# Kernel optimization log

Measured on AMD Instinct MI355X. Metric: run time of the kernel, lower is better.

## Reference

```python
import jax, jax.numpy as jnp
import numpy as np

N, E = 50000, 800000
DIM_IN, DIM_H, DIM_OUT, HEADS = 128, 32, 16, 4
HID = DIM_H * HEADS  # 128
FINAL = DIM_OUT * HEADS  # 64
NEG_SLOPE = 0.2


def _glorot(key, shape):
    fan_in, fan_out = shape[0], shape[-1] if len(shape) > 1 else shape[0]
    lim = jnp.sqrt(6.0 / (fan_in + fan_out)).astype(jnp.float32)
    return jax.random.uniform(key, shape, jnp.float32, -lim, lim)


def setup_inputs() -> dict:
    key = jax.random.key(0)
    ks = jax.random.split(key, 16)
    x = jax.random.normal(ks[0], (N, DIM_IN), jnp.float32)
    edge_index = jax.random.randint(ks[1], (2, E), 0, N, dtype=jnp.int64)
    inp = {"x": x, "edge_index": edge_index}
    # layer 1: DIM_IN -> HEADS*DIM_H
    inp["Wl1"] = _glorot(ks[2], (DIM_IN, HEADS * DIM_H))
    inp["Wr1"] = _glorot(ks[3], (DIM_IN, HEADS * DIM_H))
    inp["att1"] = _glorot(ks[4], (HEADS, DIM_H))
    inp["b1"] = jnp.zeros((HEADS * DIM_H,), jnp.float32)
    # layer 2: HID -> HEADS*DIM_H
    inp["Wl2"] = _glorot(ks[5], (HID, HEADS * DIM_H))
    inp["Wr2"] = _glorot(ks[6], (HID, HEADS * DIM_H))
    inp["att2"] = _glorot(ks[7], (HEADS, DIM_H))
    inp["b2"] = jnp.zeros((HEADS * DIM_H,), jnp.float32)
    # layer 3: HID -> HEADS*DIM_OUT
    inp["Wl3"] = _glorot(ks[8], (HID, HEADS * DIM_OUT))
    inp["Wr3"] = _glorot(ks[9], (HID, HEADS * DIM_OUT))
    inp["att3"] = _glorot(ks[10], (HEADS, DIM_OUT))
    inp["b3"] = jnp.zeros((HEADS * DIM_OUT,), jnp.float32)
    return inp


def gatv2_conv(x, src, dst, Wl, Wr, att, b, heads, ch):
    n = x.shape[0]
    xl = (x @ Wl).reshape(n, heads, ch)  # source-side transform
    xr = (x @ Wr).reshape(n, heads, ch)  # target-side transform
    m = xl[src] + xr[dst]                 # [E, H, C]
    e = jnp.einsum('ehc,hc->eh', jax.nn.leaky_relu(m, NEG_SLOPE), att)
    # segment softmax over incoming edges of each dst node
    emax = jax.ops.segment_max(e, dst, num_segments=n)
    ex = jnp.exp(e - emax[dst])
    denom = jax.ops.segment_sum(ex, dst, num_segments=n)
    alpha = ex / denom[dst]               # [E, H]
    out = jax.ops.segment_sum(alpha[:, :, None] * xl[src], dst, num_segments=n)
    return out.reshape(n, heads * ch) + b


def reference(x, edge_index, Wl1, Wr1, att1, b1, Wl2, Wr2, att2, b2, Wl3, Wr3, att3, b3):
    n = x.shape[0]
    loops = jnp.arange(n, dtype=edge_index.dtype)
    src = jnp.concatenate([edge_index[0], loops])  # PyG add_self_loops=True
    dst = jnp.concatenate([edge_index[1], loops])
    # dropout is identity in eval mode
    h = jax.nn.elu(gatv2_conv(x, src, dst, Wl1, Wr1, att1, b1, HEADS, DIM_H))
    h = jax.nn.elu(gatv2_conv(h, src, dst, Wl2, Wr2, att2, b2, HEADS, DIM_H))
    h = gatv2_conv(h, src, dst, Wl3, Wr3, att3, b3, HEADS, DIM_OUT)
    return jax.nn.log_softmax(h, axis=1)
```

## Files before the change

kernel.cpp:

```cpp
#include <hip/hip_runtime.h>
#include <math.h>

constexpr int DIN  = 128;
constexpr int FSH  = 8;
constexpr int NFBM = 200;
constexpr int LCAP = 72;
constexpr int RND  = 4096;
constexpr int FCAP = 4608;

typedef __attribute__((ext_vector_type(8))) short short8;
typedef __attribute__((ext_vector_type(4))) float f32x4;

__device__ __forceinline__ unsigned short f2bf(float f) {
  unsigned u = __float_as_uint(f);
  u = (u + 0x7FFF + ((u >> 16) & 1)) >> 16;
  return (unsigned short)u;
}
__device__ __forceinline__ float bflo(unsigned u) { return __uint_as_float(u << 16); }
__device__ __forceinline__ float bfhi(unsigned u) { return __uint_as_float(u & 0xFFFF0000u); }

__device__ __forceinline__ void unpack8(uint4 u, float* x) {
  x[0] = bflo(u.x); x[1] = bfhi(u.x); x[2] = bflo(u.y); x[3] = bfhi(u.y);
  x[4] = bflo(u.z); x[5] = bfhi(u.z); x[6] = bflo(u.w); x[7] = bfhi(u.w);
}
__device__ __forceinline__ void unpack4(uint2 u, float* x) {
  x[0] = bflo(u.x); x[1] = bfhi(u.x); x[2] = bflo(u.y); x[3] = bfhi(u.y);
}

typedef const __attribute__((address_space(1))) unsigned int guint_t;
typedef __attribute__((address_space(3))) unsigned int luint_t;
__device__ __forceinline__ void async16(const void* g, void* l) {
  __builtin_amdgcn_global_load_lds((guint_t*)g, (luint_t*)l, 16, 0, 0);
}


__global__ __launch_bounds__(256) void prep_kernel(const int* __restrict__ ei,
    int* __restrict__ gcnt, unsigned* __restrict__ gpairs, int E, int nfb, int appb,
    const float* __restrict__ Wl1, const float* __restrict__ Wr1,
    const float* __restrict__ Wl2, const float* __restrict__ Wr2,
    const float* __restrict__ Wl3, const float* __restrict__ Wr3,
    unsigned short* __restrict__ Wt) {
  __shared__ unsigned buf[NFBM * LCAP];
  __shared__ int cnt[NFBM];
  __shared__ int gbase[NFBM];
  const int tid = threadIdx.x;

  if (blockIdx.x >= appb) {
    int e = (blockIdx.x - appb) * 256 + tid;
    if (e >= 81920) return;
    const float* src; int N; int off;
    if (e < 65536) {
      int m = e >> 14; off = e & 16383; N = 128;
      src = (m == 0) ? Wl1 : (m == 1) ? Wr1 : (m == 2) ? Wl2 : Wr2;
    } else {
      int e2 = e - 65536; int m = e2 >> 13; off = e2 & 8191; N = 64;
      src = m ? Wr3 : Wl3;
    }
    int nn = off >> 7, k = off & 127;
    Wt[e] = f2bf(src[(size_t)k * N + nn]);
    return;
  }

  if (tid < NFBM) cnt[tid] = 0;
  __syncthreads();

  const int k0 = blockIdx.x * RND;
  for (int i = tid; i < RND; i += 256) {
    int k = k0 + i;
    if (k >= E) break;
    int src = ei[k], dst = ei[E + k];
    int fb = dst >> FSH;
    int pos = atomicAdd(&cnt[fb], 1);
    if (pos < LCAP)
      buf[fb * LCAP + pos] = (unsigned)src | ((unsigned)(dst & ((1 << FSH) - 1)) << 16);
  }
  __syncthreads();

  if (tid < nfb) gbase[tid] = atomicAdd(&gcnt[tid], min(cnt[tid], LCAP));
  __syncthreads();

  const int wid = tid >> 6, lane = tid & 63;
  for (int fb = wid; fb < nfb; fb += 4) {
    int c  = min(cnt[fb], LCAP);
    int gb = gbase[fb];
    if (gb >= FCAP) continue;
    c = min(c, FCAP - gb);
    unsigned* dstp = gpairs + (size_t)fb * FCAP + gb;
    const unsigned* srcp = &buf[fb * LCAP];
    for (int i = lane; i < c; i += 64) dstp[i] = srcp[i];
  }
}


struct BuildSmem { int hist[1 << FSH]; int wsum[4]; int base_s; };

__device__ __forceinline__ void build_body(BuildSmem& s, int b,
    const unsigned* __restrict__ gpairs, const int* __restrict__ gcnt,
    int* __restrict__ row_ptr, unsigned short* __restrict__ edge_src,
    int n, int nfb) {
  const int tid = threadIdx.x;
  const int lane = tid & 63, wid = tid >> 6;

  const int d0 = b << FSH;
  const int nvalid = min(1 << FSH, n - d0);

  if (wid == 0) {
    int term = 0;
    for (int i = lane; i < b; i += 64)
      term += min(gcnt[i], FCAP) + min(1 << FSH, n - (i << FSH));
#pragma unroll
    for (int o = 32; o >= 1; o >>= 1) term += __shfl_xor(term, o, 64);
    if (lane == 0) s.base_s = term;
  }
  s.hist[tid] = (tid < nvalid) ? 1 : 0;
  __syncthreads();

  const int cnt = min(gcnt[b], FCAP);
  const unsigned* bp = gpairs + (size_t)b * FCAP;
  for (int i = tid; i < cnt; i += 256)
    atomicAdd(&s.hist[bp[i] >> 16], 1);
  __syncthreads();

  const int h = s.hist[tid];
  int incl = h;
#pragma unroll
  for (int o = 1; o < 64; o <<= 1) {
    int t = __shfl_up(incl, o, 64);
    if (lane >= o) incl += t;
  }
  if (lane == 63) s.wsum[wid] = incl;
  __syncthreads();
  int wo = 0;
  for (int wq = 0; wq < wid; ++wq) wo += s.wsum[wq];
  const int base = s.base_s;
  const int excl = wo + incl - h;
  if (tid < nvalid) {
    row_ptr[d0 + tid] = base + excl;
    edge_src[base + excl] = (unsigned short)(d0 + tid);
    s.hist[tid] = excl + 1;
  } else if (d0 + tid == n) {
    row_ptr[n] = base + excl;
  }
  if (b == nfb - 1 && d0 + (1 << FSH) <= n && tid == 0)
    row_ptr[n] = base + cnt + nvalid;
  __syncthreads();

  for (int i = tid; i < cnt; i += 256) {
    unsigned p = bp[i];
    int pos = atomicAdd(&s.hist[p >> 16], 1);
    edge_src[base + pos] = (unsigned short)(p & 0xFFFFu);
  }
}


template<int NC, bool CVT>
__device__ __forceinline__ void gemm2_body(char* lds, int bid, const void* __restrict__ Ap,
    const unsigned short* __restrict__ Wlt, const unsigned short* __restrict__ Wrt,
    unsigned short* __restrict__ outl, unsigned short* __restrict__ outr, int M) {
  constexpr int WNB = NC / 16;
  char* As = lds;
  char* Ws = lds + 16384;
  const int tid  = threadIdx.x;
  const int w    = tid >> 6, lane = tid & 63;
  const int q    = lane >> 4, r15 = lane & 15;
  const int row0 = bid * 64;

  if constexpr (CVT) {
    const float* Af = (const float*)Ap;
    for (int idx = tid * 4; idx < 64 * 128; idx += 1024) {
      int rl = idx >> 7, k = idx & 127;
      int rg = row0 + rl; if (rg >= M) rg = M - 1;
      float4 v = *(const float4*)&Af[(size_t)rg * 128 + k];
      uint2 pk;
      pk.x = (unsigned)f2bf(v.x) | ((unsigned)f2bf(v.y) << 16);
      pk.y = (unsigned)f2bf(v.z) | ((unsigned)f2bf(v.w) << 16);
      char* addr = As + (rl >> 4) * 4096 + (k >> 5) * 1024 +
                   ((((k >> 3) & 3) * 16) + (rl & 15)) * 16 + (k & 7) * 2;
      *(uint2*)addr = pk;
    }
  } else {
    const unsigned short* A = (const unsigned short*)Ap;
    int r = row0 + w * 16 + r15; if (r >= M) r = M - 1;
    const char* g = (const char*)A + (size_t)r * 256 + q * 16;
    char* l = As + w * 4096;
#pragma unroll
    for (int kk = 0; kk < 4; ++kk) async16(g + kk * 64, l + kk * 1024);
  }
  for (int nt = w; nt < WNB; nt += 4) {
    const char* g = (const char*)Wlt + ((size_t)(nt * 16 + r15)) * 256 + q * 16;
    char* l = Ws + nt * 4096;
#pragma unroll
    for (int kk = 0; kk < 4; ++kk) async16(g + kk * 64, l + kk * 1024);
  }
  __syncthreads();

  const char* aw = As + w * 4096;
  f32x4 acc[WNB] = {};
#pragma unroll
  for (int kk = 0; kk < 4; ++kk) {
    short8 af = *(const short8*)(aw + kk * 1024 + (size_t)lane * 16);
#pragma unroll
    for (int nt = 0; nt < WNB; ++nt) {
      short8 bf = *(const short8*)(Ws + (nt * 4 + kk) * 1024 + (size_t)lane * 16);
      acc[nt] = __builtin_amdgcn_mfma_f32_16x16x32_bf16(af, bf, acc[nt], 0, 0, 0);
    }
  }
  {
    int rowb = row0 + w * 16 + q * 4;
#pragma unroll
    for (int nt = 0; nt < WNB; ++nt)
#pragma unroll
      for (int r = 0; r < 4; ++r) {
        int rr = rowb + r;
        if (rr < M) outl[(size_t)rr * NC + nt * 16 + r15] = f2bf(acc[nt][r]);
      }
  }
  __syncthreads();
  for (int nt = w; nt < WNB; nt += 4) {
    const char* g = (const char*)Wrt + ((size_t)(nt * 16 + r15)) * 256 + q * 16;
    char* l = Ws + nt * 4096;
#pragma unroll
    for (int kk = 0; kk < 4; ++kk) async16(g + kk * 64, l + kk * 1024);
  }
  __syncthreads();

  f32x4 acc2[WNB] = {};
#pragma unroll
  for (int kk = 0; kk < 4; ++kk) {
    short8 af = *(const short8*)(aw + kk * 1024 + (size_t)lane * 16);
#pragma unroll
    for (int nt = 0; nt < WNB; ++nt) {
      short8 bf = *(const short8*)(Ws + (nt * 4 + kk) * 1024 + (size_t)lane * 16);
      acc2[nt] = __builtin_amdgcn_mfma_f32_16x16x32_bf16(af, bf, acc2[nt], 0, 0, 0);
    }
  }
  {
    int rowb = row0 + w * 16 + q * 4;
#pragma unroll
    for (int nt = 0; nt < WNB; ++nt)
#pragma unroll
      for (int r = 0; r < 4; ++r) {
        int rr = rowb + r;
        if (rr < M) outr[(size_t)rr * NC + nt * 16 + r15] = f2bf(acc2[nt][r]);
      }
  }
}


union GemmBuildSmem { char lds[16384 + 128 * 256]; BuildSmem b; };

__global__ __launch_bounds__(256) void gemm1_build_kernel(const void* __restrict__ Ap,
    const unsigned short* __restrict__ Wlt, const unsigned short* __restrict__ Wrt,
    unsigned short* __restrict__ outl, unsigned short* __restrict__ outr,
    const unsigned* __restrict__ gpairs, const int* __restrict__ gcnt,
    int* __restrict__ row_ptr, unsigned short* __restrict__ edge_src,
    int n, int nfb) {
  __shared__ GemmBuildSmem smem;
  if (blockIdx.x < (unsigned)nfb)
    build_body(smem.b, blockIdx.x, gpairs, gcnt, row_ptr, edge_src, n, nfb);
  else
    gemm2_body<128, true>(smem.lds, blockIdx.x - nfb, Ap, Wlt, Wrt, outl, outr, n);
}


__device__ __forceinline__ uint4 agg128_node(
    const unsigned short* __restrict__ xl, const unsigned short* xr,
    const float* __restrict__ att, const float* __restrict__ bias,
    const int* __restrict__ row_ptr, const unsigned short* __restrict__ edge_src,
    int node, int c0) {
  float xrv[8];
  unpack8(*(const uint4*)&xr[(size_t)node * 128 + c0], xrv);
  float a6[8], a4[8];
  {
    float4 aa = *(const float4*)&att[c0];
    float4 ab = *(const float4*)&att[c0 + 4];
    float at[8] = {aa.x, aa.y, aa.z, aa.w, ab.x, ab.y, ab.z, ab.w};
#pragma unroll
    for (int j = 0; j < 8; ++j) { a6[j] = 0.6f * at[j]; a4[j] = 0.4f * at[j]; }
  }

  float l = 0.f, o[8] = {};
  int idx = row_ptr[node];
  const int end = row_ptr[node + 1];

  int s0 = 0, s1 = 0, s2 = 0, s3 = 0;
  if (idx + 4 <= end) {
    s0 = edge_src[idx];     s1 = edge_src[idx + 1];
    s2 = edge_src[idx + 2]; s3 = edge_src[idx + 3];
  }
  while (idx + 4 <= end) {
    uint4 u0 = *(const uint4*)&xl[(size_t)s0 * 128 + c0];
    uint4 u1 = *(const uint4*)&xl[(size_t)s1 * 128 + c0];
    uint4 u2 = *(const uint4*)&xl[(size_t)s2 * 128 + c0];
    uint4 u3 = *(const uint4*)&xl[(size_t)s3 * 128 + c0];
    idx += 4;
    if (idx + 4 <= end) {
      s0 = edge_src[idx];     s1 = edge_src[idx + 1];
      s2 = edge_src[idx + 2]; s3 = edge_src[idx + 3];
    }
    float x0[8], x1[8], x2[8], x3[8];
    unpack8(u0, x0); unpack8(u1, x1); unpack8(u2, x2); unpack8(u3, x3);
    float p0 = 0.f, p1 = 0.f, p2 = 0.f, p3 = 0.f;
#pragma unroll
    for (int j = 0; j < 8; ++j) {
      float t0 = x0[j] + xrv[j], t1 = x1[j] + xrv[j];
      float t2 = x2[j] + xrv[j], t3 = x3[j] + xrv[j];
      p0 = fmaf(t0, a6[j], p0); p0 = fmaf(fabsf(t0), a4[j], p0);
      p1 = fmaf(t1, a6[j], p1); p1 = fmaf(fabsf(t1), a4[j], p1);
      p2 = fmaf(t2, a6[j], p2); p2 = fmaf(fabsf(t2), a4[j], p2);
      p3 = fmaf(t3, a6[j], p3); p3 = fmaf(fabsf(t3), a4[j], p3);
    }
    p0 += __shfl_xor(p0, 1, 64); p0 += __shfl_xor(p0, 2, 64);
    p1 += __shfl_xor(p1, 1, 64); p1 += __shfl_xor(p1, 2, 64);
    p2 += __shfl_xor(p2, 1, 64); p2 += __shfl_xor(p2, 2, 64);
    p3 += __shfl_xor(p3, 1, 64); p3 += __shfl_xor(p3, 2, 64);
    float e0 = __expf(fminf(p0, 80.f)), e1 = __expf(fminf(p1, 80.f));
    float e2 = __expf(fminf(p2, 80.f)), e3 = __expf(fminf(p3, 80.f));
    l += (e0 + e1) + (e2 + e3);
#pragma unroll
    for (int j = 0; j < 8; ++j)
      o[j] = fmaf(e0, x0[j], fmaf(e1, x1[j], fmaf(e2, x2[j], fmaf(e3, x3[j], o[j]))));
  }
  for (; idx < end; ++idx) {
    int s = edge_src[idx];
    uint4 u0 = *(const uint4*)&xl[(size_t)s * 128 + c0];
    float x0[8];
    unpack8(u0, x0);
    float p0 = 0.f;
#pragma unroll
    for (int j = 0; j < 8; ++j) {
      float t = x0[j] + xrv[j];
      p0 = fmaf(t, a6[j], p0); p0 = fmaf(fabsf(t), a4[j], p0);
    }
    p0 += __shfl_xor(p0, 1, 64); p0 += __shfl_xor(p0, 2, 64);
    float e0 = __expf(fminf(p0, 80.f));
    l += e0;
#pragma unroll
    for (int j = 0; j < 8; ++j) o[j] = fmaf(e0, x0[j], o[j]);
  }

  float4 b0 = *(const float4*)&bias[c0];
  float4 b1 = *(const float4*)&bias[c0 + 4];
  float bb[8] = {b0.x, b0.y, b0.z, b0.w, b1.x, b1.y, b1.z, b1.w};
  float rl = 1.f / l;
  unsigned short res[8];
#pragma unroll
  for (int j = 0; j < 8; ++j) {
    float v = o[j] * rl + bb[j];
    v = v > 0.f ? v : __expf(v) - 1.f;
    res[j] = f2bf(v);
  }
  uint4 ov;
  ov.x = (unsigned)res[0] | ((unsigned)res[1] << 16);
  ov.y = (unsigned)res[2] | ((unsigned)res[3] << 16);
  ov.z = (unsigned)res[4] | ((unsigned)res[5] << 16);
  ov.w = (unsigned)res[6] | ((unsigned)res[7] << 16);
  return ov;
}


template<int NC>
__global__ __launch_bounds__(512, 4) void agg_gemm_kernel(
    const unsigned short* __restrict__ xg,
    const unsigned short* xr,
    const float* __restrict__ att, const float* __restrict__ bias,
    const int* __restrict__ row_ptr, const unsigned short* __restrict__ edge_src,
    const unsigned short* __restrict__ Wlt, const unsigned short* __restrict__ Wrt,
    unsigned short* outl, unsigned short* outr, int n) {
  constexpr int WNB = NC / 16;
  constexpr int NT2 = WNB / 2;
  __shared__ char lds[16384 + NC * 256];
  char* As = lds;
  char* Ws = lds + 16384;
  const int tid  = threadIdx.x;
  const int w8   = tid >> 6, lane = tid & 63;
  const int q    = lane >> 4, r15 = lane & 15;
  const int row0 = blockIdx.x * 64;

  for (int nt = w8; nt < WNB; nt += 8) {
    const char* g = (const char*)Wlt + ((size_t)(nt * 16 + r15)) * 256 + q * 16;
    char* l = Ws + nt * 4096;
#pragma unroll
    for (int kk = 0; kk < 4; ++kk) async16(g + kk * 64, l + kk * 1024);
  }

  const int r   = tid & 15;
  const int g16 = tid >> 4;
  const int c0  = r * 8;
#pragma unroll
  for (int pass = 0; pass < 2; ++pass) {
    const int rl   = pass * 32 + g16;
    const int node = row0 + rl;
    uint4 ov = make_uint4(0, 0, 0, 0);
    if (node < n)
      ov = agg128_node(xg, xr, att, bias, row_ptr, edge_src, node, c0);
    char* addr = As + (rl >> 4) * 4096 + (r >> 2) * 1024 +
                 (((r & 3) * 16) + (rl & 15)) * 16;
    *(uint4*)addr = ov;
  }
  __syncthreads();

  const int wq = w8 & 3;
  const int nh = w8 >> 2;
  const char* aw = As + wq * 4096;
  const int rowb = row0 + wq * 16 + q * 4;

  {
    f32x4 acc[NT2] = {};
#pragma unroll
    for (int kk = 0; kk < 4; ++kk) {
      short8 af = *(const short8*)(aw + kk * 1024 + (size_t)lane * 16);
#pragma unroll
      for (int t = 0; t < NT2; ++t) {
        short8 bf = *(const short8*)(Ws + ((nh * NT2 + t) * 4 + kk) * 1024 + (size_t)lane * 16);
        acc[t] = __builtin_amdgcn_mfma_f32_16x16x32_bf16(af, bf, acc[t], 0, 0, 0);
      }
    }
#pragma unroll
    for (int t = 0; t < NT2; ++t)
#pragma unroll
      for (int rr4 = 0; rr4 < 4; ++rr4) {
        int rr = rowb + rr4;
        if (rr < n) outl[(size_t)rr * NC + (nh * NT2 + t) * 16 + r15] = f2bf(acc[t][rr4]);
      }
  }
  __syncthreads();

  for (int nt = w8; nt < WNB; nt += 8) {
    const char* g = (const char*)Wrt + ((size_t)(nt * 16 + r15)) * 256 + q * 16;
    char* l = Ws + nt * 4096;
#pragma unroll
    for (int kk = 0; kk < 4; ++kk) async16(g + kk * 64, l + kk * 1024);
  }
  __syncthreads();

  {
    f32x4 acc[NT2] = {};
#pragma unroll
    for (int kk = 0; kk < 4; ++kk) {
      short8 af = *(const short8*)(aw + kk * 1024 + (size_t)lane * 16);
#pragma unroll
      for (int t = 0; t < NT2; ++t) {
        short8 bf = *(const short8*)(Ws + ((nh * NT2 + t) * 4 + kk) * 1024 + (size_t)lane * 16);
        acc[t] = __builtin_amdgcn_mfma_f32_16x16x32_bf16(af, bf, acc[t], 0, 0, 0);
      }
    }
#pragma unroll
    for (int t = 0; t < NT2; ++t)
#pragma unroll
      for (int rr4 = 0; rr4 < 4; ++rr4) {
        int rr = rowb + rr4;
        if (rr < n) outr[(size_t)rr * NC + (nh * NT2 + t) * 16 + r15] = f2bf(acc[t][rr4]);
      }
  }
}


__global__ __launch_bounds__(256) void aggregate64_kernel(
    const unsigned short* __restrict__ xl, const unsigned short* __restrict__ xr,
    const float* __restrict__ att, const float* __restrict__ bias,
    const int* __restrict__ row_ptr, const unsigned short* __restrict__ edge_src,
    float* __restrict__ out, int n) {
  const int tid  = threadIdx.x;
  const int r    = tid & 15;
  const int node = blockIdx.x * 16 + (tid >> 4);
  if (node >= n) return;
  const int c0 = r * 4;

  float xrv[4];
  unpack4(*(const uint2*)&xr[(size_t)node * 64 + c0], xrv);
  float a6[4], a4[4];
  {
    float4 aa = *(const float4*)&att[c0];
    float at[4] = {aa.x, aa.y, aa.z, aa.w};
#pragma unroll
    for (int j = 0; j < 4; ++j) { a6[j] = 0.6f * at[j]; a4[j] = 0.4f * at[j]; }
  }

  float l = 0.f, o[4] = {};
  int idx = row_ptr[node];
  const int end = row_ptr[node + 1];

  int s0 = 0, s1 = 0, s2 = 0, s3 = 0;
  if (idx + 4 <= end) {
    s0 = edge_src[idx];     s1 = edge_src[idx + 1];
    s2 = edge_src[idx + 2]; s3 = edge_src[idx + 3];
  }
  while (idx + 4 <= end) {
    uint2 u0 = *(const uint2*)&xl[(size_t)s0 * 64 + c0];
    uint2 u1 = *(const uint2*)&xl[(size_t)s1 * 64 + c0];
    uint2 u2 = *(const uint2*)&xl[(size_t)s2 * 64 + c0];
    uint2 u3 = *(const uint2*)&xl[(size_t)s3 * 64 + c0];
    idx += 4;
    if (idx + 4 <= end) {
      s0 = edge_src[idx];     s1 = edge_src[idx + 1];
      s2 = edge_src[idx + 2]; s3 = edge_src[idx + 3];
    }
    float x0[4], x1[4], x2[4], x3[4];
    unpack4(u0, x0); unpack4(u1, x1); unpack4(u2, x2); unpack4(u3, x3);
    float p0 = 0.f, p1 = 0.f, p2 = 0.f, p3 = 0.f;
#pragma unroll
    for (int j = 0; j < 4; ++j) {
      float t0 = x0[j] + xrv[j], t1 = x1[j] + xrv[j];
      float t2 = x2[j] + xrv[j], t3 = x3[j] + xrv[j];
      p0 = fmaf(t0, a6[j], p0); p0 = fmaf(fabsf(t0), a4[j], p0);
      p1 = fmaf(t1, a6[j], p1); p1 = fmaf(fabsf(t1), a4[j], p1);
      p2 = fmaf(t2, a6[j], p2); p2 = fmaf(fabsf(t2), a4[j], p2);
      p3 = fmaf(t3, a6[j], p3); p3 = fmaf(fabsf(t3), a4[j], p3);
    }
    p0 += __shfl_xor(p0, 1, 64); p0 += __shfl_xor(p0, 2, 64);
    p1 += __shfl_xor(p1, 1, 64); p1 += __shfl_xor(p1, 2, 64);
    p2 += __shfl_xor(p2, 1, 64); p2 += __shfl_xor(p2, 2, 64);
    p3 += __shfl_xor(p3, 1, 64); p3 += __shfl_xor(p3, 2, 64);
    float e0 = __expf(fminf(p0, 80.f)), e1 = __expf(fminf(p1, 80.f));
    float e2 = __expf(fminf(p2, 80.f)), e3 = __expf(fminf(p3, 80.f));
    l += (e0 + e1) + (e2 + e3);
#pragma unroll
    for (int j = 0; j < 4; ++j)
      o[j] = fmaf(e0, x0[j], fmaf(e1, x1[j], fmaf(e2, x2[j], fmaf(e3, x3[j], o[j]))));
  }
  for (; idx < end; ++idx) {
    int s = edge_src[idx];
    uint2 u0 = *(const uint2*)&xl[(size_t)s * 64 + c0];
    float x0[4];
    unpack4(u0, x0);
    float p0 = 0.f;
#pragma unroll
    for (int j = 0; j < 4; ++j) {
      float t = x0[j] + xrv[j];
      p0 = fmaf(t, a6[j], p0); p0 = fmaf(fabsf(t), a4[j], p0);
    }
    p0 += __shfl_xor(p0, 1, 64); p0 += __shfl_xor(p0, 2, 64);
    float e0 = __expf(fminf(p0, 80.f));
    l += e0;
#pragma unroll
    for (int j = 0; j < 4; ++j) o[j] = fmaf(e0, x0[j], o[j]);
  }

  float4 bv = *(const float4*)&bias[c0];
  float bb[4] = {bv.x, bv.y, bv.z, bv.w};
  float rl = 1.f / l;
  float rr[4];
#pragma unroll
  for (int j = 0; j < 4; ++j) rr[j] = o[j] * rl + bb[j];

  float mx = fmaxf(fmaxf(rr[0], rr[1]), fmaxf(rr[2], rr[3]));
#pragma unroll
  for (int off = 1; off < 16; off <<= 1) mx = fmaxf(mx, __shfl_xor(mx, off, 64));
  float se = __expf(rr[0] - mx) + __expf(rr[1] - mx) +
             __expf(rr[2] - mx) + __expf(rr[3] - mx);
#pragma unroll
  for (int off = 1; off < 16; off <<= 1) se += __shfl_xor(se, off, 64);
  float ls = mx + __logf(se);
  *(float4*)&out[(size_t)node * 64 + c0] =
      make_float4(rr[0] - ls, rr[1] - ls, rr[2] - ls, rr[3] - ls);
}


extern "C" void kernel_launch(void* const* d_in, const int* in_sizes, int n_in,
                              void* d_out, int out_size, void* d_ws, size_t ws_size,
                              hipStream_t stream) {
  const float* x    = (const float*)d_in[0];
  const int*   ei   = (const int*)d_in[1];
  const float* Wl1  = (const float*)d_in[2];
  const float* Wr1  = (const float*)d_in[3];
  const float* att1 = (const float*)d_in[4];
  const float* b1   = (const float*)d_in[5];
  const float* Wl2  = (const float*)d_in[6];
  const float* Wr2  = (const float*)d_in[7];
  const float* att2 = (const float*)d_in[8];
  const float* b2   = (const float*)d_in[9];
  const float* Wl3  = (const float*)d_in[10];
  const float* Wr3  = (const float*)d_in[11];
  const float* att3 = (const float*)d_in[12];
  const float* b3   = (const float*)d_in[13];
  const int n = in_sizes[0] / DIN;
  const int E = in_sizes[1] / 2;
  float* out = (float*)d_out;

  const int nfb  = (n + (1 << FSH) - 1) >> FSH;
  const int appb = (E + RND - 1) / RND;

  unsigned short* xl = (unsigned short*)d_ws;
  unsigned short* xr = xl + (size_t)n * 128;
  unsigned short* h  = xr + (size_t)n * 128;
  unsigned short* Wt = h + (size_t)n * 128;
  unsigned short* Wl1t = Wt, *Wr1t = Wt + 16384;
  unsigned short* Wl2t = Wt + 32768, *Wr2t = Wt + 49152;
  unsigned short* Wl3t = Wt + 65536, *Wr3t = Wt + 73728;
  int* row_ptr  = (int*)(Wt + 81920);
  int* gcnt     = row_ptr + (n + 16);
  unsigned short* edge_src = (unsigned short*)(gcnt + NFBM);
  unsigned* gpairs = (unsigned*)((char*)edge_src +
      ((((size_t)(E + n) * 2) + 15) & ~(size_t)15));

  hipMemsetAsync(gcnt, 0, NFBM * sizeof(int), stream);

  prep_kernel<<<appb + 320, 256, 0, stream>>>(ei, gcnt, gpairs, E, nfb, appb,
                                              Wl1, Wr1, Wl2, Wr2, Wl3, Wr3, Wt);

  const int gb = (n + 63) / 64;
  const int ab = (n + 15) / 16;

  gemm1_build_kernel<<<nfb + gb, 256, 0, stream>>>(x, Wl1t, Wr1t, xl, xr,
                                                   gpairs, gcnt, row_ptr, edge_src, n, nfb);

  agg_gemm_kernel<128><<<gb, 512, 0, stream>>>(xl, xr, att1, b1, row_ptr, edge_src,
                                               Wl2t, Wr2t, h, xr, n);

  agg_gemm_kernel<64><<<gb, 512, 0, stream>>>(h, xr, att2, b2, row_ptr, edge_src,
                                              Wl3t, Wr3t, xl, xl + (size_t)n * 64, n);

  aggregate64_kernel<<<ab, 256, 0, stream>>>(xl, xl + (size_t)n * 64, att3, b3,
                                             row_ptr, edge_src, out, n);
}
```

Before: 265.8 us.

## Partition edges by source range and aggregate range-by-range for cache locality

The CSR build now buckets each destination block's edges into three source-index ranges, so every node's edge list is ordered by source range. The aggregation kernels walk these ranges in order, with the self loop handled first, so concurrent waves tend to gather from the same slice of xl and keep it in cache. The old prefetch of edge indices is removed and the per-bucket capacities are smaller, which adds overflow risk and extra branches at range boundaries.

New measurement: 348.1 us. +31.0%, slower.

```diff
diff --git a/kernel.cpp b/kernel.cpp
--- a/kernel.cpp
+++ b/kernel.cpp
@@ -1,12 +1,15 @@
 #include <hip/hip_runtime.h>
 #include <math.h>
 
-constexpr int DIN  = 128;
-constexpr int FSH  = 8;
-constexpr int NFBM = 200;
-constexpr int LCAP = 72;
-constexpr int RND  = 4096;
-constexpr int FCAP = 4608;
+constexpr int DIN   = 128;
+constexpr int FSH   = 8;
+constexpr int NFBM  = 200;
+constexpr int NRG   = 3;
+constexpr int RB1   = 16672;
+constexpr int RB2   = 33344;
+constexpr int LCAP2 = 28;
+constexpr int RND   = 4096;
+constexpr int FCAPR = 1664;
 
 typedef __attribute__((ext_vector_type(8))) short short8;
 typedef __attribute__((ext_vector_type(4))) float f32x4;
@@ -40,9 +43,9 @@
     const float* __restrict__ Wl2, const float* __restrict__ Wr2,
     const float* __restrict__ Wl3, const float* __restrict__ Wr3,
     unsigned short* __restrict__ Wt) {
-  __shared__ unsigned buf[NFBM * LCAP];
-  __shared__ int cnt[NFBM];
-  __shared__ int gbase[NFBM];
+  __shared__ unsigned buf[NFBM * NRG * LCAP2];
+  __shared__ int cnt[NFBM * NRG];
+  __shared__ int gbase[NFBM * NRG];
   const int tid = threadIdx.x;
 
   if (blockIdx.x >= appb) {
@@ -61,7 +64,7 @@
     return;
   }
 
-  if (tid < NFBM) cnt[tid] = 0;
+  for (int i = tid; i < NFBM * NRG; i += 256) cnt[i] = 0;
   __syncthreads();
 
   const int k0 = blockIdx.x * RND;
@@ -69,24 +72,26 @@
     int k = k0 + i;
     if (k >= E) break;
     int src = ei[k], dst = ei[E + k];
-    int fb = dst >> FSH;
-    int pos = atomicAdd(&cnt[fb], 1);
-    if (pos < LCAP)
-      buf[fb * LCAP + pos] = (unsigned)src | ((unsigned)(dst & ((1 << FSH) - 1)) << 16);
-  }
-  __syncthreads();
-
-  if (tid < nfb) gbase[tid] = atomicAdd(&gcnt[tid], min(cnt[tid], LCAP));
+    int rg = (src >= RB1) + (src >= RB2);
+    int slot = (dst >> FSH) * NRG + rg;
+    int pos = atomicAdd(&cnt[slot], 1);
+    if (pos < LCAP2)
+      buf[slot * LCAP2 + pos] = (unsigned)src | ((unsigned)(dst & ((1 << FSH) - 1)) << 16);
+  }
+  __syncthreads();
+
+  for (int i = tid; i < nfb * NRG; i += 256)
+    gbase[i] = atomicAdd(&gcnt[i], min(cnt[i], LCAP2));
   __syncthreads();
 
   const int wid = tid >> 6, lane = tid & 63;
-  for (int fb = wid; fb < nfb; fb += 4) {
-    int c  = min(cnt[fb], LCAP);
-    int gb = gbase[fb];
-    if (gb >= FCAP) continue;
-    c = min(c, FCAP - gb);
-    unsigned* dstp = gpairs + (size_t)fb * FCAP + gb;
-    const unsigned* srcp = &buf[fb * LCAP];
+  for (int slot = wid; slot < nfb * NRG; slot += 4) {
+    int c  = min(cnt[slot], LCAP2);
+    int gb = gbase[slot];
+    if (gb >= FCAPR) continue;
+    c = min(c, FCAPR - gb);
+    unsigned* dstp = gpairs + (size_t)slot * FCAPR + gb;
+    const unsigned* srcp = &buf[slot * LCAP2];
     for (int i = lane; i < c; i += 64) dstp[i] = srcp[i];
   }
 }
@@ -106,8 +111,8 @@
 
   if (wid == 0) {
     int term = 0;
-    for (int i = lane; i < b; i += 64)
-      term += min(gcnt[i], FCAP) + min(1 << FSH, n - (i << FSH));
+    for (int i = lane; i < b * NRG; i += 64) term += min(gcnt[i], FCAPR);
+    for (int i = lane; i < b; i += 64) term += min(1 << FSH, n - (i << FSH));
 #pragma unroll
     for (int o = 32; o >= 1; o >>= 1) term += __shfl_xor(term, o, 64);
     if (lane == 0) s.base_s = term;
@@ -115,10 +120,17 @@
   s.hist[tid] = (tid < nvalid) ? 1 : 0;
   __syncthreads();
 
-  const int cnt = min(gcnt[b], FCAP);
-  const unsigned* bp = gpairs + (size_t)b * FCAP;
-  for (int i = tid; i < cnt; i += 256)
-    atomicAdd(&s.hist[bp[i] >> 16], 1);
+  int cs0 = min(gcnt[b * NRG + 0], FCAPR);
+  int cs1 = min(gcnt[b * NRG + 1], FCAPR);
+  int cs2 = min(gcnt[b * NRG + 2], FCAPR);
+  const int cntTotal = cs0 + cs1 + cs2;
+#pragma unroll
+  for (int rg = 0; rg < NRG; ++rg) {
+    int c = (rg == 0) ? cs0 : (rg == 1) ? cs1 : cs2;
+    const unsigned* bp = gpairs + (size_t)(b * NRG + rg) * FCAPR;
+    for (int i = tid; i < c; i += 256)
+      atomicAdd(&s.hist[bp[i] >> 16], 1);
+  }
   __syncthreads();
 
   const int h = s.hist[tid];
@@ -142,13 +154,19 @@
     row_ptr[n] = base + excl;
   }
   if (b == nfb - 1 && d0 + (1 << FSH) <= n && tid == 0)
-    row_ptr[n] = base + cnt + nvalid;
-  __syncthreads();
-
-  for (int i = tid; i < cnt; i += 256) {
-    unsigned p = bp[i];
-    int pos = atomicAdd(&s.hist[p >> 16], 1);
-    edge_src[base + pos] = (unsigned short)(p & 0xFFFFu);
+    row_ptr[n] = base + cntTotal + nvalid;
+  __syncthreads();
+
+#pragma unroll
+  for (int rg = 0; rg < NRG; ++rg) {
+    int c = (rg == 0) ? cs0 : (rg == 1) ? cs1 : cs2;
+    const unsigned* bp = gpairs + (size_t)(b * NRG + rg) * FCAPR;
+    for (int i = tid; i < c; i += 256) {
+      unsigned p = bp[i];
+      int pos = atomicAdd(&s.hist[p >> 16], 1);
+      edge_src[base + pos] = (unsigned short)(p & 0xFFFFu);
+    }
+    __syncthreads();
   }
 }
 
@@ -280,24 +298,10 @@
   }
 
   float l = 0.f, o[8] = {};
-  int idx = row_ptr[node];
-  const int end = row_ptr[node + 1];
-
-  int s0 = 0, s1 = 0, s2 = 0, s3 = 0;
-  if (idx + 4 <= end) {
-    s0 = edge_src[idx];     s1 = edge_src[idx + 1];
-    s2 = edge_src[idx + 2]; s3 = edge_src[idx + 3];
-  }
-  while (idx + 4 <= end) {
-    uint4 u0 = *(const uint4*)&xl[(size_t)s0 * 128 + c0];
-    uint4 u1 = *(const uint4*)&xl[(size_t)s1 * 128 + c0];
-    uint4 u2 = *(const uint4*)&xl[(size_t)s2 * 128 + c0];
-    uint4 u3 = *(const uint4*)&xl[(size_t)s3 * 128 + c0];
-    idx += 4;
-    if (idx + 4 <= end) {
-      s0 = edge_src[idx];     s1 = edge_src[idx + 1];
-      s2 = edge_src[idx + 2]; s3 = edge_src[idx + 3];
-    }
+
+  auto ld = [&](int s) -> uint4 { return *(const uint4*)&xl[(size_t)s * 128 + c0]; };
+
+  auto edge4 = [&](uint4 u0, uint4 u1, uint4 u2, uint4 u3) {
     float x0[8], x1[8], x2[8], x3[8];
     unpack8(u0, x0); unpack8(u1, x1); unpack8(u2, x2); unpack8(u3, x3);
     float p0 = 0.f, p1 = 0.f, p2 = 0.f, p3 = 0.f;
@@ -320,10 +324,9 @@
 #pragma unroll
     for (int j = 0; j < 8; ++j)
       o[j] = fmaf(e0, x0[j], fmaf(e1, x1[j], fmaf(e2, x2[j], fmaf(e3, x3[j], o[j]))));
-  }
-  for (; idx < end; ++idx) {
-    int s = edge_src[idx];
-    uint4 u0 = *(const uint4*)&xl[(size_t)s * 128 + c0];
+  };
+
+  auto edge1 = [&](uint4 u0) {
     float x0[8];
     unpack8(u0, x0);
     float p0 = 0.f;
@@ -337,6 +340,29 @@
     l += e0;
 #pragma unroll
     for (int j = 0; j < 8; ++j) o[j] = fmaf(e0, x0[j], o[j]);
+  };
+
+  edge1(ld(node));
+  int idx = row_ptr[node] + 1;
+  const int end = row_ptr[node + 1];
+
+#pragma unroll 1
+  for (int p = 0; p < NRG; ++p) {
+    const int hi = (p == 0) ? RB1 : (p == 1) ? RB2 : 0x7fffffff;
+    while (idx + 4 <= end) {
+      int s0 = edge_src[idx],     s1 = edge_src[idx + 1];
+      int s2 = edge_src[idx + 2], s3 = edge_src[idx + 3];
+      if (s3 >= hi) break;
+      uint4 u0 = ld(s0), u1 = ld(s1), u2 = ld(s2), u3 = ld(s3);
+      idx += 4;
+      edge4(u0, u1, u2, u3);
+    }
+    while (idx < end) {
+      int s = edge_src[idx];
+      if (s >= hi) break;
+      edge1(ld(s));
+      ++idx;
+    }
   }
 
   float4 b0 = *(const float4*)&bias[c0];
@@ -478,24 +504,10 @@
   }
 
   float l = 0.f, o[4] = {};
-  int idx = row_ptr[node];
-  const int end = row_ptr[node + 1];
-
-  int s0 = 0, s1 = 0, s2 = 0, s3 = 0;
-  if (idx + 4 <= end) {
-    s0 = edge_src[idx];     s1 = edge_src[idx + 1];
-    s2 = edge_src[idx + 2]; s3 = edge_src[idx + 3];
-  }
-  while (idx + 4 <= end) {
-    uint2 u0 = *(const uint2*)&xl[(size_t)s0 * 64 + c0];
-    uint2 u1 = *(const uint2*)&xl[(size_t)s1 * 64 + c0];
-    uint2 u2 = *(const uint2*)&xl[(size_t)s2 * 64 + c0];
-    uint2 u3 = *(const uint2*)&xl[(size_t)s3 * 64 + c0];
-    idx += 4;
-    if (idx + 4 <= end) {
-      s0 = edge_src[idx];     s1 = edge_src[idx + 1];
-      s2 = edge_src[idx + 2]; s3 = edge_src[idx + 3];
-    }
+
+  auto ld = [&](int s) -> uint2 { return *(const uint2*)&xl[(size_t)s * 64 + c0]; };
+
+  auto edge4 = [&](uint2 u0, uint2 u1, uint2 u2, uint2 u3) {
     float x0[4], x1[4], x2[4], x3[4];
     unpack4(u0, x0); unpack4(u1, x1); unpack4(u2, x2); unpack4(u3, x3);
     float p0 = 0.f, p1 = 0.f, p2 = 0.f, p3 = 0.f;
@@ -518,10 +530,9 @@
 #pragma unroll
     for (int j = 0; j < 4; ++j)
       o[j] = fmaf(e0, x0[j], fmaf(e1, x1[j], fmaf(e2, x2[j], fmaf(e3, x3[j], o[j]))));
-  }
-  for (; idx < end; ++idx) {
-    int s = edge_src[idx];
-    uint2 u0 = *(const uint2*)&xl[(size_t)s * 64 + c0];
+  };
+
+  auto edge1 = [&](uint2 u0) {
     float x0[4];
     unpack4(u0, x0);
     float p0 = 0.f;
@@ -535,6 +546,29 @@
     l += e0;
 #pragma unroll
     for (int j = 0; j < 4; ++j) o[j] = fmaf(e0, x0[j], o[j]);
+  };
+
+  edge1(ld(node));
+  int idx = row_ptr[node] + 1;
+  const int end = row_ptr[node + 1];
+
+#pragma unroll 1
+  for (int p = 0; p < NRG; ++p) {
+    const int hi = (p == 0) ? RB1 : (p == 1) ? RB2 : 0x7fffffff;
+    while (idx + 4 <= end) {
+      int s0 = edge_src[idx],     s1 = edge_src[idx + 1];
+      int s2 = edge_src[idx + 2], s3 = edge_src[idx + 3];
+      if (s3 >= hi) break;
+      uint2 u0 = ld(s0), u1 = ld(s1), u2 = ld(s2), u3 = ld(s3);
+      idx += 4;
+      edge4(u0, u1, u2, u3);
+    }
+    while (idx < end) {
+      int s = edge_src[idx];
+      if (s >= hi) break;
+      edge1(ld(s));
+      ++idx;
+    }
   }
 
   float4 bv = *(const float4*)&bias[c0];
@@ -590,11 +624,11 @@
   unsigned short* Wl3t = Wt + 65536, *Wr3t = Wt + 73728;
   int* row_ptr  = (int*)(Wt + 81920);
   int* gcnt     = row_ptr + (n + 16);
-  unsigned short* edge_src = (unsigned short*)(gcnt + NFBM);
+  unsigned short* edge_src = (unsigned short*)(gcnt + NFBM * NRG);
   unsigned* gpairs = (unsigned*)((char*)edge_src +
       ((((size_t)(E + n) * 2) + 15) & ~(size_t)15));
 
-  hipMemsetAsync(gcnt, 0, NFBM * sizeof(int), stream);
+  hipMemsetAsync(gcnt, 0, NFBM * NRG * sizeof(int), stream);
 
   prep_kernel<<<appb + 320, 256, 0, stream>>>(ei, gcnt, gpairs, E, nfb, appb,
                                               Wl1, Wr1, Wl2, Wr2, Wl3, Wr3, Wt);
```

## Degree-sort nodes within blocks to balance per-thread aggregation work

Applied to the files above, without the earlier changes.

Inside each aggregation block, node degrees are loaded, ranked by a small O(64^2) LDS sort, and threads take nodes in a serpentine order. Pass 0 takes the low ranks and pass 1 the high ranks, so each 16-lane group's total edge count evens out. The final aggregate kernel becomes a two-pass loop over 32 nodes per block with the same balancing. This targets imbalance from varying in-degree across the node groups sharing a wavefront, at the cost of extra syncs, a serial rank loop and fewer blocks for the last kernel.

New measurement: 262.6 us. Within noise of the previous version (-1.2%).

```diff
diff --git a/kernel.cpp b/kernel.cpp
--- a/kernel.cpp
+++ b/kernel.cpp
@@ -370,6 +370,8 @@
   constexpr int WNB = NC / 16;
   constexpr int NT2 = WNB / 2;
   __shared__ char lds[16384 + NC * 256];
+  __shared__ int deg[64];
+  __shared__ int perm[64];
   char* As = lds;
   char* Ws = lds + 16384;
   const int tid  = threadIdx.x;
@@ -383,13 +385,29 @@
 #pragma unroll
     for (int kk = 0; kk < 4; ++kk) async16(g + kk * 64, l + kk * 1024);
   }
+  if (tid < 64) {
+    int nd = row0 + tid;
+    deg[tid] = (nd < n) ? (row_ptr[nd + 1] - row_ptr[nd]) : 0;
+  }
+  __syncthreads();
+  if (tid < 64) {
+    int d = deg[tid], rk = 0;
+#pragma unroll 1
+    for (int j = 0; j < 64; ++j) {
+      int dj = deg[j];
+      rk += (dj < d) || (dj == d && j < tid);
+    }
+    perm[rk] = tid;
+  }
+  __syncthreads();
 
   const int r   = tid & 15;
   const int g16 = tid >> 4;
   const int c0  = r * 8;
 #pragma unroll
   for (int pass = 0; pass < 2; ++pass) {
-    const int rl   = pass * 32 + g16;
+    const int rank = pass ? (63 - g16) : g16;
+    const int rl   = perm[rank];
     const int node = row0 + rl;
     uint4 ov = make_uint4(0, 0, 0, 0);
     if (node < n)
@@ -456,17 +474,11 @@
 }
 
 
-__global__ __launch_bounds__(256) void aggregate64_kernel(
+__device__ __forceinline__ void agg64_node(
     const unsigned short* __restrict__ xl, const unsigned short* __restrict__ xr,
     const float* __restrict__ att, const float* __restrict__ bias,
     const int* __restrict__ row_ptr, const unsigned short* __restrict__ edge_src,
-    float* __restrict__ out, int n) {
-  const int tid  = threadIdx.x;
-  const int r    = tid & 15;
-  const int node = blockIdx.x * 16 + (tid >> 4);
-  if (node >= n) return;
-  const int c0 = r * 4;
-
+    float* __restrict__ out, int node, int c0) {
   float xrv[4];
   unpack4(*(const uint2*)&xr[(size_t)node * 64 + c0], xrv);
   float a6[4], a4[4];
@@ -554,6 +566,44 @@
   float ls = mx + __logf(se);
   *(float4*)&out[(size_t)node * 64 + c0] =
       make_float4(rr[0] - ls, rr[1] - ls, rr[2] - ls, rr[3] - ls);
+}
+
+__global__ __launch_bounds__(256) void aggregate64_kernel(
+    const unsigned short* __restrict__ xl, const unsigned short* __restrict__ xr,
+    const float* __restrict__ att, const float* __restrict__ bias,
+    const int* __restrict__ row_ptr, const unsigned short* __restrict__ edge_src,
+    float* __restrict__ out, int n) {
+  __shared__ int deg[32];
+  __shared__ int perm[32];
+  const int tid  = threadIdx.x;
+  const int r    = tid & 15;
+  const int g16  = tid >> 4;
+  const int row0 = blockIdx.x * 32;
+
+  if (tid < 32) {
+    int nd = row0 + tid;
+    deg[tid] = (nd < n) ? (row_ptr[nd + 1] - row_ptr[nd]) : 0;
+  }
+  __syncthreads();
+  if (tid < 32) {
+    int d = deg[tid], rk = 0;
+#pragma unroll 1
+    for (int j = 0; j < 32; ++j) {
+      int dj = deg[j];
+      rk += (dj < d) || (dj == d && j < tid);
+    }
+    perm[rk] = tid;
+  }
+  __syncthreads();
+
+  const int c0 = r * 4;
+#pragma unroll
+  for (int pass = 0; pass < 2; ++pass) {
+    const int rank = pass ? (31 - g16) : g16;
+    const int node = row0 + perm[rank];
+    if (node < n)
+      agg64_node(xl, xr, att, bias, row_ptr, edge_src, out, node, c0);
+  }
 }
 
 
@@ -600,7 +650,7 @@
                                               Wl1, Wr1, Wl2, Wr2, Wl3, Wr3, Wt);
 
   const int gb = (n + 63) / 64;
-  const int ab = (n + 15) / 16;
+  const int ab = (n + 31) / 32;
 
   gemm1_build_kernel<<<nfb + gb, 256, 0, stream>>>(x, Wl1t, Wr1t, xl, xr,
                                                    gpairs, gcnt, row_ptr, edge_src, n, nfb);
```
